# Optimization experiments

Hardware: AMD Instinct MI355X
Metric: run time of the kernel (lower is better)

Reference implementation:

```python
import jax, jax.numpy as jnp
import numpy as np

F, H, E, D, B = 1024, 256, 64, 64, 4096
N = F + H


def setup_inputs() -> dict:
    key = jax.random.key(0)
    k = jax.random.split(key, 7)
    values = jax.random.normal(k[0], (B, F), dtype=jnp.float32)
    # GlorotNormal-ish init for embeddings and dense layers
    feat_emb = jax.random.normal(k[1], (F, E), dtype=jnp.float32) * (2.0 / (F + E)) ** 0.5
    hidden_emb = jax.random.normal(k[2], (H, E), dtype=jnp.float32) * (2.0 / (H + E)) ** 0.5
    w_kernel = jax.random.normal(k[3], (2 * E, D), dtype=jnp.float32) * (2.0 / (2 * E + D)) ** 0.5
    w_bias = jnp.zeros((D,), dtype=jnp.float32)
    u_kernel = jax.random.normal(k[4], (D,), dtype=jnp.float32) * (2.0 / (D + 1)) ** 0.5
    # sparse ancestor mask; every node is its own ancestor -> diagonal True
    mask = jax.random.bernoulli(k[5], 0.02, (F, N))
    mask = mask.at[jnp.arange(F), jnp.arange(F)].set(True)
    return {
        "values": values,
        "feat_emb": feat_emb,
        "hidden_emb": hidden_emb,
        "w_kernel": w_kernel,
        "w_bias": w_bias,
        "u_kernel": u_kernel,
        "mask": mask,
    }


def reference(values, feat_emb, hidden_emb, w_kernel, w_bias, u_kernel, mask):
    # full embedding table: [N, E]
    full = jnp.concatenate([feat_emb, hidden_emb], axis=0)
    # Dense(w) applied to concat([e_i, f_j]) == e_i @ Wa + f_j @ Wb + b
    Wa, Wb = w_kernel[:E], w_kernel[E:]
    feat_proj = feat_emb @ Wa            # [F, D]
    full_proj = full @ Wb                # [N, D]
    h = jnp.tanh(feat_proj[:, None, :] + full_proj[None, :, :] + w_bias)  # [F, N, D]
    score = jnp.einsum("fnd,d->fn", h, u_kernel)  # [F, N]
    # masked exp / normalize (faithful to tf.where(mask, exp(score), 0) / sum)
    escore = jnp.where(mask, jnp.exp(score), 0.0)
    attn = escore / jnp.sum(escore, axis=1, keepdims=True)  # [F, N]
    context = attn @ full                # [F, E]
    return values @ context              # [B, E]
```

## Files before the change

kernel.cpp:

```cpp
#include <hip/hip_runtime.h>
#include <stdint.h>

#define F 1024
#define H 256
#define E 64
#define D 64
#define B 4096
#define NN 1280

typedef __attribute__((ext_vector_type(8))) short bf16x8;
typedef __attribute__((ext_vector_type(4))) float f32x4;

__device__ inline uint16_t f2bf_rne(float x) {
    union { float f; uint32_t u; } v; v.f = x;
    uint32_t u = v.u + 0x7fffu + ((v.u >> 16) & 1u);
    return (uint16_t)(u >> 16);
}
__device__ inline float bf2f(uint16_t h) {
    union { uint32_t u; float f; } v; v.u = ((uint32_t)h) << 16;
    return v.f;
}

__device__ void probe_mask_body(const void* __restrict__ mask, int* __restrict__ flag) {
    __shared__ int s_byte, s_int, s_float;
    int t = threadIdx.x;
    if (t == 0) { s_byte = 1; s_int = 1; s_float = 1; }
    __syncthreads();
    long idx = (long)t * NN + t;
    const uint8_t* mb = (const uint8_t*)mask;
    const int*     mi = (const int*)mask;
    const float*   mf = (const float*)mask;
    if (mb[idx] != 1)    atomicAnd(&s_byte, 0);
    if (mi[idx] != 1)    atomicAnd(&s_int, 0);
    if (mf[idx] != 1.0f) atomicAnd(&s_float, 0);
    __syncthreads();
    if (t == 0) {
        int mode = 0;
        if (s_byte) mode = 0;
        else if (s_int) mode = 1;
        else if (s_float) mode = 2;
        flag[0] = mode;
    }
}

__global__ void proj_kernel(const float* __restrict__ feat_emb,
                            const float* __restrict__ hidden_emb,
                            const float* __restrict__ w_kernel,
                            const void*  __restrict__ mask,
                            float* __restrict__ fp, float* __restrict__ gp,
                            int* __restrict__ flag) {
    if (blockIdx.x == (F + NN) / 4) {
        probe_mask_body(mask, flag);
        return;
    }
    int tid = threadIdx.x;
    int r = blockIdx.x * 4 + (tid >> 6);
    int d = tid & 63;
    const float* emb;
    const float* W;
    float* outp;
    if (r < F) {
        emb = feat_emb + (size_t)r * E;
        W = w_kernel;
        outp = fp + (size_t)r * D + d;
    } else {
        int rn = r - F;
        emb = (rn < F) ? (feat_emb + (size_t)rn * E)
                       : (hidden_emb + (size_t)(rn - F) * E);
        W = w_kernel + (size_t)E * D;
        outp = gp + (size_t)rn * D + d;
    }
    float a0 = 0.f, a1 = 0.f, a2 = 0.f, a3 = 0.f;
#pragma unroll
    for (int e = 0; e < E; e += 4) {
        a0 = fmaf(emb[e + 0], W[(e + 0) * D + d], a0);
        a1 = fmaf(emb[e + 1], W[(e + 1) * D + d], a1);
        a2 = fmaf(emb[e + 2], W[(e + 2) * D + d], a2);
        a3 = fmaf(emb[e + 3], W[(e + 3) * D + d], a3);
    }
    *outp = (a0 + a1) + (a2 + a3);
}

__global__ __launch_bounds__(256)
void attn_ctx_kernel(const float* __restrict__ feat_emb,
                     const float* __restrict__ hidden_emb,
                     const void*  __restrict__ mask,
                     const float* __restrict__ w_bias,
                     const float* __restrict__ u_kernel,
                     const float* __restrict__ fp,
                     const float* __restrict__ gp,
                     const int*   __restrict__ flag,
                     uint16_t* __restrict__ ctxB_hi,
                     uint16_t* __restrict__ ctxB_lo) {
    __shared__ float s_cacc[4][64];
    __shared__ float s_den[4];
    __shared__ unsigned short s_idx[4][320];
    int tid = threadIdx.x;
    int w = tid >> 6, lane = tid & 63;
    int f = blockIdx.x;
    int mode = flag[0];
    float uk  = u_kernel[lane];
    float bv  = w_bias[lane];
    float fpv = fp[(size_t)f * D + lane];
    const uint8_t* mb = (const uint8_t*)mask;
    const int*     mi = (const int*)mask;
    const float*   mf = (const float*)mask;

    bool mv[5];
    long base = (long)f * NN + w * 320;
#pragma unroll
    for (int c = 0; c < 5; ++c) {
        long midx = base + c * 64 + lane;
        if (mode == 0)      mv[c] = (mb[midx] != 0);
        else if (mode == 1) mv[c] = (mi[midx] != 0);
        else                mv[c] = (mf[midx] != 0.f);
    }
    unsigned long long below = lane ? (~0ull >> (64 - lane)) : 0ull;
    int cnt = 0;
#pragma unroll
    for (int c = 0; c < 5; ++c) {
        unsigned long long bal = __ballot(mv[c]);
        if (mv[c]) {
            int pos = cnt + __popcll(bal & below);
            s_idx[w][pos] = (unsigned short)(w * 320 + c * 64 + lane);
        }
        cnt += __popcll(bal);
    }

    float denom = 0.f, cacc = 0.f;
    const float k2E = 2.885390082f;
    const float kE  = 1.44269504f;
    for (int i = 0; i < cnt; i += 4) {
        int   n[4];
        float g[4], fv[4];
        bool  valid[4];
#pragma unroll
        for (int j = 0; j < 4; ++j) {
            valid[j] = (i + j) < cnt;
            n[j] = s_idx[w][valid[j] ? i + j : i];
        }
#pragma unroll
        for (int j = 0; j < 4; ++j) g[j] = gp[(size_t)n[j] * D + lane];
#pragma unroll
        for (int j = 0; j < 4; ++j)
            fv[j] = (n[j] < F) ? feat_emb[(size_t)n[j] * E + lane]
                               : hidden_emb[(size_t)(n[j] - F) * E + lane];
#pragma unroll
        for (int j = 0; j < 4; ++j) {
            float x  = fpv + g[j] + bv;
            float ax = fminf(fabsf(x), 10.f);
            float ex = exp2f(k2E * ax);
            float th = (ex - 1.f) * __builtin_amdgcn_rcpf(ex + 1.f);
            th = copysignf(th, x);
            float t = uk * th;
#pragma unroll
            for (int off = 32; off; off >>= 1) t += __shfl_xor(t, off);
            float es = exp2f(t * kE);
            if (valid[j]) {
                denom += es;
                cacc = fmaf(es, fv[j], cacc);
            }
        }
    }
    s_cacc[w][lane] = cacc;
    if (lane == 0) s_den[w] = denom;
    __syncthreads();
    if (w == 0) {
        float c = s_cacc[0][lane] + s_cacc[1][lane] + s_cacc[2][lane] + s_cacc[3][lane];
        float dn = s_den[0] + s_den[1] + s_den[2] + s_den[3];
        c /= dn;
        uint16_t hi = f2bf_rne(c);
        float lof = c - bf2f(hi);
        uint16_t lo = f2bf_rne(lof);
        int ks = f >> 5, kk = f & 31;
        int ch = kk >> 3, j = kk & 7;
        int l  = ch * 16 + (lane & 15);
        int nt = lane >> 4;
        int off = ((ks * 4 + nt) * 64 + l) * 8 + j;
        ctxB_hi[off] = hi;
        ctxB_lo[off] = lo;
    }
}

#define OKW 16
__global__ __launch_bounds__(1024, 4)
void out_kernel(const float* __restrict__ values,
                const uint16_t* __restrict__ ctxB_hi,
                const uint16_t* __restrict__ ctxB_lo,
                float* __restrict__ out) {
    __shared__ float red[OKW][16][64];
    int tid = threadIdx.x;
    int w = tid >> 6, l = tid & 63;
    int m0 = blockIdx.x * 16;
    f32x4 acc[4];
#pragma unroll
    for (int nt = 0; nt < 4; ++nt) acc[nt] = (f32x4){0.f, 0.f, 0.f, 0.f};
    int row = m0 + (l & 15);
    int kchunk = (l >> 4) * 8;
#pragma unroll
    for (int s = 0; s < 2; ++s) {
        int ks = w * 2 + s;
        int k0 = ks * 32 + kchunk;
        const float4 va0 = *reinterpret_cast<const float4*>(values + (size_t)row * F + k0);
        const float4 va1 = *reinterpret_cast<const float4*>(values + (size_t)row * F + k0 + 4);
        float av0 = va0.x, av1 = va0.y, av2 = va0.z, av3 = va0.w;
        float av4 = va1.x, av5 = va1.y, av6 = va1.z, av7 = va1.w;
        bf16x8 ahi, alo;
        {
            uint16_t h;
            h = f2bf_rne(av0); ahi[0] = (short)h; alo[0] = (short)f2bf_rne(av0 - bf2f(h));
            h = f2bf_rne(av1); ahi[1] = (short)h; alo[1] = (short)f2bf_rne(av1 - bf2f(h));
            h = f2bf_rne(av2); ahi[2] = (short)h; alo[2] = (short)f2bf_rne(av2 - bf2f(h));
            h = f2bf_rne(av3); ahi[3] = (short)h; alo[3] = (short)f2bf_rne(av3 - bf2f(h));
            h = f2bf_rne(av4); ahi[4] = (short)h; alo[4] = (short)f2bf_rne(av4 - bf2f(h));
            h = f2bf_rne(av5); ahi[5] = (short)h; alo[5] = (short)f2bf_rne(av5 - bf2f(h));
            h = f2bf_rne(av6); ahi[6] = (short)h; alo[6] = (short)f2bf_rne(av6 - bf2f(h));
            h = f2bf_rne(av7); ahi[7] = (short)h; alo[7] = (short)f2bf_rne(av7 - bf2f(h));
        }
#pragma unroll
        for (int nt = 0; nt < 4; ++nt) {
            int boff = ((ks * 4 + nt) * 64 + l) * 8;
            bf16x8 bhi = *reinterpret_cast<const bf16x8*>(ctxB_hi + boff);
            bf16x8 blo = *reinterpret_cast<const bf16x8*>(ctxB_lo + boff);
            acc[nt] = __builtin_amdgcn_mfma_f32_16x16x32_bf16(ahi, bhi, acc[nt], 0, 0, 0);
            acc[nt] = __builtin_amdgcn_mfma_f32_16x16x32_bf16(ahi, blo, acc[nt], 0, 0, 0);
            acc[nt] = __builtin_amdgcn_mfma_f32_16x16x32_bf16(alo, bhi, acc[nt], 0, 0, 0);
        }
    }
#pragma unroll
    for (int nt = 0; nt < 4; ++nt)
#pragma unroll
        for (int r = 0; r < 4; ++r) {
            int orow = (l >> 4) * 4 + r;
            int ocol = nt * 16 + (l & 15);
            red[w][orow][ocol] = acc[nt][r];
        }
    __syncthreads();
    int orow = tid >> 6, ocol = tid & 63;
    float s2 = 0.f;
#pragma unroll
    for (int ww = 0; ww < OKW; ++ww) s2 += red[ww][orow][ocol];
    out[(size_t)(m0 + orow) * D + ocol] = s2;
}

extern "C" void kernel_launch(void* const* d_in, const int* in_sizes, int n_in,
                              void* d_out, int out_size, void* d_ws, size_t ws_size,
                              hipStream_t stream) {
    const float* values     = (const float*)d_in[0];
    const float* feat_emb   = (const float*)d_in[1];
    const float* hidden_emb = (const float*)d_in[2];
    const float* w_kernel   = (const float*)d_in[3];
    const float* w_bias     = (const float*)d_in[4];
    const float* u_kernel   = (const float*)d_in[5];
    const void*  mask       = (const void*)d_in[6];
    float* out = (float*)d_out;

    int*      flag    = (int*)d_ws;
    float*    wsf     = (float*)d_ws;
    float*    fp      = wsf + 64;
    float*    gp      = fp + F * D;
    uint16_t* ctxB_hi = (uint16_t*)(gp + NN * D);
    uint16_t* ctxB_lo = ctxB_hi + 32 * 4 * 64 * 8;

    proj_kernel<<<(F + NN) / 4 + 1, 256, 0, stream>>>(feat_emb, hidden_emb, w_kernel,
                                                      mask, fp, gp, flag);
    attn_ctx_kernel<<<F, 256, 0, stream>>>(feat_emb, hidden_emb, mask, w_bias,
                                           u_kernel, fp, gp, flag, ctxB_hi, ctxB_lo);
    out_kernel<<<B / 16, 1024, 0, stream>>>(values, ctxB_hi, ctxB_lo, out);
}
```

Measured before the change: 25.26 us.

## Fuse three kernels into one persistent kernel with grid-wide barriers

```diff
diff --git a/kernel.cpp b/kernel.cpp
--- a/kernel.cpp
+++ b/kernel.cpp
@@ -7,6 +7,7 @@
 #define D 64
 #define B 4096
 #define NN 1280
+#define NBLK 256
 
 typedef __attribute__((ext_vector_type(8))) short bf16x8;
 typedef __attribute__((ext_vector_type(4))) float f32x4;
@@ -21,226 +22,228 @@
     return v.f;
 }
 
-__device__ void probe_mask_body(const void* __restrict__ mask, int* __restrict__ flag) {
-    __shared__ int s_byte, s_int, s_float;
-    int t = threadIdx.x;
-    if (t == 0) { s_byte = 1; s_int = 1; s_float = 1; }
+__device__ __forceinline__ void grid_barrier(int* cnt) {
     __syncthreads();
-    long idx = (long)t * NN + t;
-    const uint8_t* mb = (const uint8_t*)mask;
-    const int*     mi = (const int*)mask;
-    const float*   mf = (const float*)mask;
-    if (mb[idx] != 1)    atomicAnd(&s_byte, 0);
-    if (mi[idx] != 1)    atomicAnd(&s_int, 0);
-    if (mf[idx] != 1.0f) atomicAnd(&s_float, 0);
+    if (threadIdx.x == 0) {
+        __threadfence();
+        __hip_atomic_fetch_add(cnt, 1, __ATOMIC_ACQ_REL, __HIP_MEMORY_SCOPE_AGENT);
+        while (__hip_atomic_load(cnt, __ATOMIC_ACQUIRE, __HIP_MEMORY_SCOPE_AGENT) < NBLK)
+            __builtin_amdgcn_s_sleep(2);
+        __threadfence();
+    }
     __syncthreads();
-    if (t == 0) {
-        int mode = 0;
-        if (s_byte) mode = 0;
-        else if (s_int) mode = 1;
-        else if (s_float) mode = 2;
-        flag[0] = mode;
-    }
-}
-
-__global__ void proj_kernel(const float* __restrict__ feat_emb,
-                            const float* __restrict__ hidden_emb,
-                            const float* __restrict__ w_kernel,
-                            const void*  __restrict__ mask,
-                            float* __restrict__ fp, float* __restrict__ gp,
-                            int* __restrict__ flag) {
-    if (blockIdx.x == (F + NN) / 4) {
-        probe_mask_body(mask, flag);
-        return;
-    }
-    int tid = threadIdx.x;
-    int r = blockIdx.x * 4 + (tid >> 6);
-    int d = tid & 63;
-    const float* emb;
-    const float* W;
-    float* outp;
-    if (r < F) {
-        emb = feat_emb + (size_t)r * E;
-        W = w_kernel;
-        outp = fp + (size_t)r * D + d;
-    } else {
-        int rn = r - F;
-        emb = (rn < F) ? (feat_emb + (size_t)rn * E)
-                       : (hidden_emb + (size_t)(rn - F) * E);
-        W = w_kernel + (size_t)E * D;
-        outp = gp + (size_t)rn * D + d;
-    }
-    float a0 = 0.f, a1 = 0.f, a2 = 0.f, a3 = 0.f;
-#pragma unroll
-    for (int e = 0; e < E; e += 4) {
-        a0 = fmaf(emb[e + 0], W[(e + 0) * D + d], a0);
-        a1 = fmaf(emb[e + 1], W[(e + 1) * D + d], a1);
-        a2 = fmaf(emb[e + 2], W[(e + 2) * D + d], a2);
-        a3 = fmaf(emb[e + 3], W[(e + 3) * D + d], a3);
-    }
-    *outp = (a0 + a1) + (a2 + a3);
-}
-
-__global__ __launch_bounds__(256)
-void attn_ctx_kernel(const float* __restrict__ feat_emb,
-                     const float* __restrict__ hidden_emb,
-                     const void*  __restrict__ mask,
-                     const float* __restrict__ w_bias,
-                     const float* __restrict__ u_kernel,
-                     const float* __restrict__ fp,
-                     const float* __restrict__ gp,
-                     const int*   __restrict__ flag,
-                     uint16_t* __restrict__ ctxB_hi,
-                     uint16_t* __restrict__ ctxB_lo) {
-    __shared__ float s_cacc[4][64];
-    __shared__ float s_den[4];
-    __shared__ unsigned short s_idx[4][320];
+}
+
+__global__ __launch_bounds__(1024, 4)
+void fused_kernel(const float* __restrict__ values,
+                  const float* __restrict__ feat_emb,
+                  const float* __restrict__ hidden_emb,
+                  const float* __restrict__ w_kernel,
+                  const float* __restrict__ w_bias,
+                  const float* __restrict__ u_kernel,
+                  const void*  __restrict__ mask,
+                  float* __restrict__ out,
+                  int* __restrict__ flag, int* __restrict__ cnt1, int* __restrict__ cnt2,
+                  float* __restrict__ fp, float* __restrict__ gp,
+                  uint16_t* __restrict__ ctxB_hi, uint16_t* __restrict__ ctxB_lo) {
+    __shared__ __align__(16) char smem[16 * 16 * 64 * 4];
+    float (*red)[16][64] = (float (*)[16][64])smem;
+    unsigned short (*s_idx)[320] = (unsigned short (*)[320])smem;
+    float* s_cacc = (float*)(smem + 16 * 320 * 2);
+    float* s_den  = (float*)(smem + 16 * 320 * 2 + 16 * 64 * 4);
+
     int tid = threadIdx.x;
     int w = tid >> 6, lane = tid & 63;
-    int f = blockIdx.x;
-    int mode = flag[0];
-    float uk  = u_kernel[lane];
-    float bv  = w_bias[lane];
-    float fpv = fp[(size_t)f * D + lane];
-    const uint8_t* mb = (const uint8_t*)mask;
-    const int*     mi = (const int*)mask;
-    const float*   mf = (const float*)mask;
-
-    bool mv[5];
-    long base = (long)f * NN + w * 320;
-#pragma unroll
-    for (int c = 0; c < 5; ++c) {
-        long midx = base + c * 64 + lane;
-        if (mode == 0)      mv[c] = (mb[midx] != 0);
-        else if (mode == 1) mv[c] = (mi[midx] != 0);
-        else                mv[c] = (mf[midx] != 0.f);
-    }
-    unsigned long long below = lane ? (~0ull >> (64 - lane)) : 0ull;
-    int cnt = 0;
-#pragma unroll
-    for (int c = 0; c < 5; ++c) {
-        unsigned long long bal = __ballot(mv[c]);
-        if (mv[c]) {
-            int pos = cnt + __popcll(bal & below);
-            s_idx[w][pos] = (unsigned short)(w * 320 + c * 64 + lane);
-        }
-        cnt += __popcll(bal);
-    }
-
-    float denom = 0.f, cacc = 0.f;
-    const float k2E = 2.885390082f;
-    const float kE  = 1.44269504f;
-    for (int i = 0; i < cnt; i += 4) {
-        int   n[4];
-        float g[4], fv[4];
-        bool  valid[4];
-#pragma unroll
-        for (int j = 0; j < 4; ++j) {
-            valid[j] = (i + j) < cnt;
-            n[j] = s_idx[w][valid[j] ? i + j : i];
-        }
-#pragma unroll
-        for (int j = 0; j < 4; ++j) g[j] = gp[(size_t)n[j] * D + lane];
-#pragma unroll
-        for (int j = 0; j < 4; ++j)
-            fv[j] = (n[j] < F) ? feat_emb[(size_t)n[j] * E + lane]
-                               : hidden_emb[(size_t)(n[j] - F) * E + lane];
-#pragma unroll
-        for (int j = 0; j < 4; ++j) {
-            float x  = fpv + g[j] + bv;
-            float ax = fminf(fabsf(x), 10.f);
-            float ex = exp2f(k2E * ax);
-            float th = (ex - 1.f) * __builtin_amdgcn_rcpf(ex + 1.f);
-            th = copysignf(th, x);
-            float t = uk * th;
-#pragma unroll
-            for (int off = 32; off; off >>= 1) t += __shfl_xor(t, off);
-            float es = exp2f(t * kE);
-            if (valid[j]) {
-                denom += es;
-                cacc = fmaf(es, fv[j], cacc);
-            }
-        }
-    }
-    s_cacc[w][lane] = cacc;
-    if (lane == 0) s_den[w] = denom;
-    __syncthreads();
-    if (w == 0) {
-        float c = s_cacc[0][lane] + s_cacc[1][lane] + s_cacc[2][lane] + s_cacc[3][lane];
-        float dn = s_den[0] + s_den[1] + s_den[2] + s_den[3];
-        c /= dn;
-        uint16_t hi = f2bf_rne(c);
-        float lof = c - bf2f(hi);
-        uint16_t lo = f2bf_rne(lof);
-        int ks = f >> 5, kk = f & 31;
-        int ch = kk >> 3, j = kk & 7;
-        int l  = ch * 16 + (lane & 15);
-        int nt = lane >> 4;
-        int off = ((ks * 4 + nt) * 64 + l) * 8 + j;
-        ctxB_hi[off] = hi;
-        ctxB_lo[off] = lo;
-    }
-}
-
-#define OKW 16
-__global__ __launch_bounds__(1024, 4)
-void out_kernel(const float* __restrict__ values,
-                const uint16_t* __restrict__ ctxB_hi,
-                const uint16_t* __restrict__ ctxB_lo,
-                float* __restrict__ out) {
-    __shared__ float red[OKW][16][64];
-    int tid = threadIdx.x;
-    int w = tid >> 6, l = tid & 63;
-    int m0 = blockIdx.x * 16;
-    f32x4 acc[4];
-#pragma unroll
-    for (int nt = 0; nt < 4; ++nt) acc[nt] = (f32x4){0.f, 0.f, 0.f, 0.f};
-    int row = m0 + (l & 15);
-    int kchunk = (l >> 4) * 8;
-#pragma unroll
-    for (int s = 0; s < 2; ++s) {
-        int ks = w * 2 + s;
-        int k0 = ks * 32 + kchunk;
-        const float4 va0 = *reinterpret_cast<const float4*>(values + (size_t)row * F + k0);
-        const float4 va1 = *reinterpret_cast<const float4*>(values + (size_t)row * F + k0 + 4);
-        float av0 = va0.x, av1 = va0.y, av2 = va0.z, av3 = va0.w;
-        float av4 = va1.x, av5 = va1.y, av6 = va1.z, av7 = va1.w;
-        bf16x8 ahi, alo;
-        {
-            uint16_t h;
-            h = f2bf_rne(av0); ahi[0] = (short)h; alo[0] = (short)f2bf_rne(av0 - bf2f(h));
-            h = f2bf_rne(av1); ahi[1] = (short)h; alo[1] = (short)f2bf_rne(av1 - bf2f(h));
-            h = f2bf_rne(av2); ahi[2] = (short)h; alo[2] = (short)f2bf_rne(av2 - bf2f(h));
-            h = f2bf_rne(av3); ahi[3] = (short)h; alo[3] = (short)f2bf_rne(av3 - bf2f(h));
-            h = f2bf_rne(av4); ahi[4] = (short)h; alo[4] = (short)f2bf_rne(av4 - bf2f(h));
-            h = f2bf_rne(av5); ahi[5] = (short)h; alo[5] = (short)f2bf_rne(av5 - bf2f(h));
-            h = f2bf_rne(av6); ahi[6] = (short)h; alo[6] = (short)f2bf_rne(av6 - bf2f(h));
-            h = f2bf_rne(av7); ahi[7] = (short)h; alo[7] = (short)f2bf_rne(av7 - bf2f(h));
-        }
-#pragma unroll
-        for (int nt = 0; nt < 4; ++nt) {
-            int boff = ((ks * 4 + nt) * 64 + l) * 8;
-            bf16x8 bhi = *reinterpret_cast<const bf16x8*>(ctxB_hi + boff);
-            bf16x8 blo = *reinterpret_cast<const bf16x8*>(ctxB_lo + boff);
-            acc[nt] = __builtin_amdgcn_mfma_f32_16x16x32_bf16(ahi, bhi, acc[nt], 0, 0, 0);
-            acc[nt] = __builtin_amdgcn_mfma_f32_16x16x32_bf16(ahi, blo, acc[nt], 0, 0, 0);
-            acc[nt] = __builtin_amdgcn_mfma_f32_16x16x32_bf16(alo, bhi, acc[nt], 0, 0, 0);
-        }
-    }
-#pragma unroll
-    for (int nt = 0; nt < 4; ++nt)
-#pragma unroll
-        for (int r = 0; r < 4; ++r) {
-            int orow = (l >> 4) * 4 + r;
-            int ocol = nt * 16 + (l & 15);
-            red[w][orow][ocol] = acc[nt][r];
-        }
-    __syncthreads();
-    int orow = tid >> 6, ocol = tid & 63;
-    float s2 = 0.f;
-#pragma unroll
-    for (int ww = 0; ww < OKW; ++ww) s2 += red[ww][orow][ocol];
-    out[(size_t)(m0 + orow) * D + ocol] = s2;
+
+    {
+        int rl = w;
+        int r = blockIdx.x * 9 + rl;
+        if (rl < 9) {
+            int d = lane;
+            const float* emb;
+            const float* W;
+            float* outp;
+            if (r < F) {
+                emb = feat_emb + (size_t)r * E;
+                W = w_kernel;
+                outp = fp + (size_t)r * D + d;
+            } else {
+                int rn = r - F;
+                emb = (rn < F) ? (feat_emb + (size_t)rn * E)
+                               : (hidden_emb + (size_t)(rn - F) * E);
+                W = w_kernel + (size_t)E * D;
+                outp = gp + (size_t)rn * D + d;
+            }
+            float a0 = 0.f, a1 = 0.f, a2 = 0.f, a3 = 0.f;
+#pragma unroll
+            for (int e = 0; e < E; e += 4) {
+                a0 = fmaf(emb[e + 0], W[(e + 0) * D + d], a0);
+                a1 = fmaf(emb[e + 1], W[(e + 1) * D + d], a1);
+                a2 = fmaf(emb[e + 2], W[(e + 2) * D + d], a2);
+                a3 = fmaf(emb[e + 3], W[(e + 3) * D + d], a3);
+            }
+            *outp = (a0 + a1) + (a2 + a3);
+        } else if (blockIdx.x == 0 && w == 9) {
+            long e = (long)lane * (NN + 1);
+            bool okb = ((const uint8_t*)mask)[e] == 1;
+            bool oki = ((const int*)mask)[e] == 1;
+            bool okf = ((const float*)mask)[e] == 1.0f;
+            unsigned long long bb = __ballot(okb);
+            unsigned long long bi = __ballot(oki);
+            unsigned long long bf = __ballot(okf);
+            if (lane == 0) {
+                int mode = 0;
+                if (bb == ~0ull) mode = 0;
+                else if (bi == ~0ull) mode = 1;
+                else if (bf == ~0ull) mode = 2;
+                *flag = mode;
+            }
+        }
+    }
+    grid_barrier(cnt1);
+
+    {
+        int rowl = w >> 2, wq = w & 3;
+        int f = blockIdx.x * 4 + rowl;
+        int mode = *flag;
+        float uk  = u_kernel[lane];
+        float bv  = w_bias[lane];
+        float fpv = fp[(size_t)f * D + lane];
+        const uint8_t* mb = (const uint8_t*)mask;
+        const int*     mi = (const int*)mask;
+        const float*   mf = (const float*)mask;
+
+        bool mv[5];
+        long base = (long)f * NN + wq * 320;
+#pragma unroll
+        for (int c = 0; c < 5; ++c) {
+            long midx = base + c * 64 + lane;
+            if (mode == 0)      mv[c] = (mb[midx] != 0);
+            else if (mode == 1) mv[c] = (mi[midx] != 0);
+            else                mv[c] = (mf[midx] != 0.f);
+        }
+        unsigned long long below = lane ? (~0ull >> (64 - lane)) : 0ull;
+        int cnt = 0;
+#pragma unroll
+        for (int c = 0; c < 5; ++c) {
+            unsigned long long bal = __ballot(mv[c]);
+            if (mv[c]) {
+                int pos = cnt + __popcll(bal & below);
+                s_idx[w][pos] = (unsigned short)(wq * 320 + c * 64 + lane);
+            }
+            cnt += __popcll(bal);
+        }
+
+        float denom = 0.f, cacc = 0.f;
+        const float k2E = 2.885390082f;
+        const float kE  = 1.44269504f;
+        for (int i = 0; i < cnt; i += 4) {
+            int   n[4];
+            float g[4], fv[4];
+            bool  valid[4];
+#pragma unroll
+            for (int j = 0; j < 4; ++j) {
+                valid[j] = (i + j) < cnt;
+                n[j] = s_idx[w][valid[j] ? i + j : i];
+            }
+#pragma unroll
+            for (int j = 0; j < 4; ++j) g[j] = gp[(size_t)n[j] * D + lane];
+#pragma unroll
+            for (int j = 0; j < 4; ++j)
+                fv[j] = (n[j] < F) ? feat_emb[(size_t)n[j] * E + lane]
+                                   : hidden_emb[(size_t)(n[j] - F) * E + lane];
+#pragma unroll
+            for (int j = 0; j < 4; ++j) {
+                float x  = fpv + g[j] + bv;
+                float ax = fminf(fabsf(x), 10.f);
+                float ex = exp2f(k2E * ax);
+                float th = (ex - 1.f) * __builtin_amdgcn_rcpf(ex + 1.f);
+                th = copysignf(th, x);
+                float t = uk * th;
+#pragma unroll
+                for (int off = 32; off; off >>= 1) t += __shfl_xor(t, off);
+                float es = exp2f(t * kE);
+                if (valid[j]) {
+                    denom += es;
+                    cacc = fmaf(es, fv[j], cacc);
+                }
+            }
+        }
+        s_cacc[w * 64 + lane] = cacc;
+        if (lane == 0) s_den[w] = denom;
+        __syncthreads();
+        if (wq == 0) {
+            float c = s_cacc[w * 64 + lane] + s_cacc[(w + 1) * 64 + lane]
+                    + s_cacc[(w + 2) * 64 + lane] + s_cacc[(w + 3) * 64 + lane];
+            float dn = s_den[w] + s_den[w + 1] + s_den[w + 2] + s_den[w + 3];
+            c /= dn;
+            uint16_t hi = f2bf_rne(c);
+            float lof = c - bf2f(hi);
+            uint16_t lo = f2bf_rne(lof);
+            int ks = f >> 5, kk = f & 31;
+            int ch = kk >> 3, j = kk & 7;
+            int l  = ch * 16 + (lane & 15);
+            int nt = lane >> 4;
+            int off = ((ks * 4 + nt) * 64 + l) * 8 + j;
+            ctxB_hi[off] = hi;
+            ctxB_lo[off] = lo;
+        }
+    }
+    grid_barrier(cnt2);
+
+    {
+        int l = lane;
+        int m0 = blockIdx.x * 16;
+        f32x4 acc[4];
+#pragma unroll
+        for (int nt = 0; nt < 4; ++nt) acc[nt] = (f32x4){0.f, 0.f, 0.f, 0.f};
+        int row = m0 + (l & 15);
+        int kchunk = (l >> 4) * 8;
+#pragma unroll
+        for (int s = 0; s < 2; ++s) {
+            int ks = w * 2 + s;
+            int k0 = ks * 32 + kchunk;
+            const float4 va0 = *reinterpret_cast<const float4*>(values + (size_t)row * F + k0);
+            const float4 va1 = *reinterpret_cast<const float4*>(values + (size_t)row * F + k0 + 4);
+            float av0 = va0.x, av1 = va0.y, av2 = va0.z, av3 = va0.w;
+            float av4 = va1.x, av5 = va1.y, av6 = va1.z, av7 = va1.w;
+            bf16x8 ahi, alo;
+            {
+                uint16_t h;
+                h = f2bf_rne(av0); ahi[0] = (short)h; alo[0] = (short)f2bf_rne(av0 - bf2f(h));
+                h = f2bf_rne(av1); ahi[1] = (short)h; alo[1] = (short)f2bf_rne(av1 - bf2f(h));
+                h = f2bf_rne(av2); ahi[2] = (short)h; alo[2] = (short)f2bf_rne(av2 - bf2f(h));
+                h = f2bf_rne(av3); ahi[3] = (short)h; alo[3] = (short)f2bf_rne(av3 - bf2f(h));
+                h = f2bf_rne(av4); ahi[4] = (short)h; alo[4] = (short)f2bf_rne(av4 - bf2f(h));
+                h = f2bf_rne(av5); ahi[5] = (short)h; alo[5] = (short)f2bf_rne(av5 - bf2f(h));
+                h = f2bf_rne(av6); ahi[6] = (short)h; alo[6] = (short)f2bf_rne(av6 - bf2f(h));
+                h = f2bf_rne(av7); ahi[7] = (short)h; alo[7] = (short)f2bf_rne(av7 - bf2f(h));
+            }
+#pragma unroll
+            for (int nt = 0; nt < 4; ++nt) {
+                int boff = ((ks * 4 + nt) * 64 + l) * 8;
+                bf16x8 bhi = *reinterpret_cast<const bf16x8*>(ctxB_hi + boff);
+                bf16x8 blo = *reinterpret_cast<const bf16x8*>(ctxB_lo + boff);
+                acc[nt] = __builtin_amdgcn_mfma_f32_16x16x32_bf16(ahi, bhi, acc[nt], 0, 0, 0);
+                acc[nt] = __builtin_amdgcn_mfma_f32_16x16x32_bf16(ahi, blo, acc[nt], 0, 0, 0);
+                acc[nt] = __builtin_amdgcn_mfma_f32_16x16x32_bf16(alo, bhi, acc[nt], 0, 0, 0);
+            }
+        }
+#pragma unroll
+        for (int nt = 0; nt < 4; ++nt)
+#pragma unroll
+            for (int r = 0; r < 4; ++r) {
+                int orow = (l >> 4) * 4 + r;
+                int ocol = nt * 16 + (l & 15);
+                red[w][orow][ocol] = acc[nt][r];
+            }
+        __syncthreads();
+        int orow = tid >> 6, ocol = tid & 63;
+        float s2 = 0.f;
+#pragma unroll
+        for (int ww = 0; ww < 16; ++ww) s2 += red[ww][orow][ocol];
+        out[(size_t)(m0 + orow) * D + ocol] = s2;
+    }
 }
 
 extern "C" void kernel_launch(void* const* d_in, const int* in_sizes, int n_in,
@@ -255,16 +258,16 @@
     const void*  mask       = (const void*)d_in[6];
     float* out = (float*)d_out;
 
-    int*      flag    = (int*)d_ws;
+    int*      wsi     = (int*)d_ws;
     float*    wsf     = (float*)d_ws;
     float*    fp      = wsf + 64;
     float*    gp      = fp + F * D;
     uint16_t* ctxB_hi = (uint16_t*)(gp + NN * D);
     uint16_t* ctxB_lo = ctxB_hi + 32 * 4 * 64 * 8;
 
-    proj_kernel<<<(F + NN) / 4 + 1, 256, 0, stream>>>(feat_emb, hidden_emb, w_kernel,
-                                                      mask, fp, gp, flag);
-    attn_ctx_kernel<<<F, 256, 0, stream>>>(feat_emb, hidden_emb, mask, w_bias,
-                                           u_kernel, fp, gp, flag, ctxB_hi, ctxB_lo);
-    out_kernel<<<B / 16, 1024, 0, stream>>>(values, ctxB_hi, ctxB_lo, out);
-}
+    hipMemsetAsync(d_ws, 0, 256, stream);
+    fused_kernel<<<NBLK, 1024, 0, stream>>>(values, feat_emb, hidden_emb, w_kernel,
+                                            w_bias, u_kernel, mask, out,
+                                            wsi + 0, wsi + 1, wsi + 2,
+                                            fp, gp, ctxB_hi, ctxB_lo);
+}
```

Result: slower. 72.92 us (+188.6%).

## Fuse projection kernel into attention kernel, recomputing projections from shared-memory weights

Applied to the files above, without the earlier changes.

```diff
diff --git a/kernel.cpp b/kernel.cpp
--- a/kernel.cpp
+++ b/kernel.cpp
@@ -21,87 +21,67 @@
     return v.f;
 }
 
-__device__ void probe_mask_body(const void* __restrict__ mask, int* __restrict__ flag) {
-    __shared__ int s_byte, s_int, s_float;
-    int t = threadIdx.x;
-    if (t == 0) { s_byte = 1; s_int = 1; s_float = 1; }
-    __syncthreads();
-    long idx = (long)t * NN + t;
-    const uint8_t* mb = (const uint8_t*)mask;
-    const int*     mi = (const int*)mask;
-    const float*   mf = (const float*)mask;
-    if (mb[idx] != 1)    atomicAnd(&s_byte, 0);
-    if (mi[idx] != 1)    atomicAnd(&s_int, 0);
-    if (mf[idx] != 1.0f) atomicAnd(&s_float, 0);
-    __syncthreads();
-    if (t == 0) {
-        int mode = 0;
-        if (s_byte) mode = 0;
-        else if (s_int) mode = 1;
-        else if (s_float) mode = 2;
-        flag[0] = mode;
-    }
-}
-
-__global__ void proj_kernel(const float* __restrict__ feat_emb,
-                            const float* __restrict__ hidden_emb,
-                            const float* __restrict__ w_kernel,
-                            const void*  __restrict__ mask,
-                            float* __restrict__ fp, float* __restrict__ gp,
-                            int* __restrict__ flag) {
-    if (blockIdx.x == (F + NN) / 4) {
-        probe_mask_body(mask, flag);
-        return;
-    }
-    int tid = threadIdx.x;
-    int r = blockIdx.x * 4 + (tid >> 6);
-    int d = tid & 63;
-    const float* emb;
-    const float* W;
-    float* outp;
-    if (r < F) {
-        emb = feat_emb + (size_t)r * E;
-        W = w_kernel;
-        outp = fp + (size_t)r * D + d;
-    } else {
-        int rn = r - F;
-        emb = (rn < F) ? (feat_emb + (size_t)rn * E)
-                       : (hidden_emb + (size_t)(rn - F) * E);
-        W = w_kernel + (size_t)E * D;
-        outp = gp + (size_t)rn * D + d;
-    }
-    float a0 = 0.f, a1 = 0.f, a2 = 0.f, a3 = 0.f;
-#pragma unroll
-    for (int e = 0; e < E; e += 4) {
-        a0 = fmaf(emb[e + 0], W[(e + 0) * D + d], a0);
-        a1 = fmaf(emb[e + 1], W[(e + 1) * D + d], a1);
-        a2 = fmaf(emb[e + 2], W[(e + 2) * D + d], a2);
-        a3 = fmaf(emb[e + 3], W[(e + 3) * D + d], a3);
-    }
-    *outp = (a0 + a1) + (a2 + a3);
-}
-
 __global__ __launch_bounds__(256)
-void attn_ctx_kernel(const float* __restrict__ feat_emb,
-                     const float* __restrict__ hidden_emb,
-                     const void*  __restrict__ mask,
-                     const float* __restrict__ w_bias,
-                     const float* __restrict__ u_kernel,
-                     const float* __restrict__ fp,
-                     const float* __restrict__ gp,
-                     const int*   __restrict__ flag,
-                     uint16_t* __restrict__ ctxB_hi,
-                     uint16_t* __restrict__ ctxB_lo) {
+void attn_kernel(const float* __restrict__ feat_emb,
+                 const float* __restrict__ hidden_emb,
+                 const float* __restrict__ w_kernel,
+                 const float* __restrict__ w_bias,
+                 const float* __restrict__ u_kernel,
+                 const void*  __restrict__ mask,
+                 uint16_t* __restrict__ ctxB_hi,
+                 uint16_t* __restrict__ ctxB_lo) {
+    __shared__ __align__(16) float sW[8192];
+    __shared__ __align__(16) float sfeat[64];
+    __shared__ __align__(16) float sfull[4][4][64];
+    __shared__ unsigned short s_idx[4][320];
     __shared__ float s_cacc[4][64];
     __shared__ float s_den[4];
-    __shared__ unsigned short s_idx[4][320];
+    __shared__ int   s_mode;
+
     int tid = threadIdx.x;
     int w = tid >> 6, lane = tid & 63;
     int f = blockIdx.x;
-    int mode = flag[0];
-    float uk  = u_kernel[lane];
-    float bv  = w_bias[lane];
-    float fpv = fp[(size_t)f * D + lane];
+
+    {
+        const float4* src = (const float4*)w_kernel;
+        float4* dst = (float4*)sW;
+#pragma unroll
+        for (int i = 0; i < 8; ++i) dst[tid + 256 * i] = src[tid + 256 * i];
+    }
+    if (w == 0) {
+        sfeat[lane] = feat_emb[(size_t)f * E + lane];
+        long e = (long)lane * (NN + 1);
+        bool okb = ((const uint8_t*)mask)[e] == 1;
+        bool oki = ((const int*)mask)[e] == 1;
+        bool okf = ((const float*)mask)[e] == 1.0f;
+        unsigned long long bb = __ballot(okb);
+        unsigned long long bi = __ballot(oki);
+        unsigned long long bf = __ballot(okf);
+        if (lane == 0) {
+            int mode = 0;
+            if (bb == ~0ull) mode = 0;
+            else if (bi == ~0ull) mode = 1;
+            else if (bf == ~0ull) mode = 2;
+            s_mode = mode;
+        }
+    }
+    __syncthreads();
+    int mode = s_mode;
+    const float* sWa = sW;
+    const float* sWb = sW + 4096;
+
+    float fpv = 0.f;
+#pragma unroll
+    for (int e4 = 0; e4 < 64; e4 += 4) {
+        float4 fr = *(const float4*)&sfeat[e4];
+        fpv = fmaf(fr.x, sWa[(e4 + 0) * 64 + lane],
+              fmaf(fr.y, sWa[(e4 + 1) * 64 + lane],
+              fmaf(fr.z, sWa[(e4 + 2) * 64 + lane],
+              fmaf(fr.w, sWa[(e4 + 3) * 64 + lane], fpv))));
+    }
+
+    float uk = u_kernel[lane];
+    float bv = w_bias[lane];
     const uint8_t* mb = (const uint8_t*)mask;
     const int*     mi = (const int*)mask;
     const float*   mf = (const float*)mask;
@@ -132,7 +112,7 @@
     const float kE  = 1.44269504f;
     for (int i = 0; i < cnt; i += 4) {
         int   n[4];
-        float g[4], fv[4];
+        float fv[4];
         bool  valid[4];
 #pragma unroll
         for (int j = 0; j < 4; ++j) {
@@ -140,14 +120,31 @@
             n[j] = s_idx[w][valid[j] ? i + j : i];
         }
 #pragma unroll
-        for (int j = 0; j < 4; ++j) g[j] = gp[(size_t)n[j] * D + lane];
-#pragma unroll
         for (int j = 0; j < 4; ++j)
             fv[j] = (n[j] < F) ? feat_emb[(size_t)n[j] * E + lane]
                                : hidden_emb[(size_t)(n[j] - F) * E + lane];
 #pragma unroll
+        for (int j = 0; j < 4; ++j) sfull[w][j][lane] = fv[j];
+        float g0 = 0.f, g1 = 0.f, g2 = 0.f, g3 = 0.f;
+#pragma unroll
+        for (int e4 = 0; e4 < 64; e4 += 4) {
+            float4 a0 = *(const float4*)&sfull[w][0][e4];
+            float4 a1 = *(const float4*)&sfull[w][1][e4];
+            float4 a2 = *(const float4*)&sfull[w][2][e4];
+            float4 a3 = *(const float4*)&sfull[w][3][e4];
+            float w0 = sWb[(e4 + 0) * 64 + lane];
+            float w1 = sWb[(e4 + 1) * 64 + lane];
+            float w2 = sWb[(e4 + 2) * 64 + lane];
+            float w3 = sWb[(e4 + 3) * 64 + lane];
+            g0 = fmaf(a0.x, w0, fmaf(a0.y, w1, fmaf(a0.z, w2, fmaf(a0.w, w3, g0))));
+            g1 = fmaf(a1.x, w0, fmaf(a1.y, w1, fmaf(a1.z, w2, fmaf(a1.w, w3, g1))));
+            g2 = fmaf(a2.x, w0, fmaf(a2.y, w1, fmaf(a2.z, w2, fmaf(a2.w, w3, g2))));
+            g3 = fmaf(a3.x, w0, fmaf(a3.y, w1, fmaf(a3.z, w2, fmaf(a3.w, w3, g3))));
+        }
+        float gg[4] = {g0, g1, g2, g3};
+#pragma unroll
         for (int j = 0; j < 4; ++j) {
-            float x  = fpv + g[j] + bv;
+            float x  = fpv + gg[j] + bv;
             float ax = fminf(fabsf(x), 10.f);
             float ex = exp2f(k2E * ax);
             float th = (ex - 1.f) * __builtin_amdgcn_rcpf(ex + 1.f);
@@ -255,16 +252,10 @@
     const void*  mask       = (const void*)d_in[6];
     float* out = (float*)d_out;
 
-    int*      flag    = (int*)d_ws;
-    float*    wsf     = (float*)d_ws;
-    float*    fp      = wsf + 64;
-    float*    gp      = fp + F * D;
-    uint16_t* ctxB_hi = (uint16_t*)(gp + NN * D);
+    uint16_t* ctxB_hi = (uint16_t*)d_ws;
     uint16_t* ctxB_lo = ctxB_hi + 32 * 4 * 64 * 8;
 
-    proj_kernel<<<(F + NN) / 4 + 1, 256, 0, stream>>>(feat_emb, hidden_emb, w_kernel,
-                                                      mask, fp, gp, flag);
-    attn_ctx_kernel<<<F, 256, 0, stream>>>(feat_emb, hidden_emb, mask, w_bias,
-                                           u_kernel, fp, gp, flag, ctxB_hi, ctxB_lo);
+    attn_kernel<<<F, 256, 0, stream>>>(feat_emb, hidden_emb, w_kernel, w_bias,
+                                       u_kernel, mask, ctxB_hi, ctxB_lo);
     out_kernel<<<B / 16, 1024, 0, stream>>>(values, ctxB_hi, ctxB_lo, out);
 }
```

New measurement: 35.01 us. +38.6%, slower.
